# Kernel optimization log

Measured on AMD Instinct MI355X. Metric: run time of the kernel, lower is better.

The kernel has to match this reference:

```python
import jax, jax.numpy as jnp
import numpy as np

THRESHOLD = 0.3          # config.sparse_threshold
COMPETITION_FACTOR = 2.0 # config.competition_factor
TARGET_SPARSITY = 0.1    # config.target_sparsity


def setup_inputs() -> dict:
    key = jax.random.key(0)
    B, D = 32768, 1024
    H = D // 4
    ks = jax.random.split(key, 18)
    def lin(k, fan_in, shape):
        return jax.random.normal(k, shape, dtype=jnp.float32) / np.sqrt(fan_in)
    return {
        "features": jax.random.normal(ks[0], (B, D), dtype=jnp.float32),
        # sparse_gating: Linear(D, D//4) -> ReLU -> Linear(D//4, D) -> Sigmoid
        "w_g1": lin(ks[1], D, (D, H)), "b_g1": jnp.zeros((H,), jnp.float32),
        "w_g2": lin(ks[2], H, (H, D)), "b_g2": jnp.zeros((D,), jnp.float32),
        # competition_calculator: Linear(D, D) -> ReLU -> Linear(D, 1) -> Sigmoid
        "w_c1": lin(ks[3], D, (D, D)), "b_c1": jnp.zeros((D,), jnp.float32),
        "w_c2": lin(ks[4], D, (D, 1)), "b_c2": jnp.zeros((1,), jnp.float32),
        # sparsity_feedback: Linear(2, 16) -> ReLU -> Linear(16, D) -> Sigmoid
        "w_r1": lin(ks[5], 2, (2, 16)), "b_r1": jnp.zeros((16,), jnp.float32),
        "w_r2": lin(ks[6], 16, (16, D)), "b_r2": jnp.zeros((D,), jnp.float32),
        # adaptive_threshold: Linear(3, 16) -> ReLU -> Linear(16, 1) -> Sigmoid
        "w_m1": lin(ks[7], 3, (3, 16)), "b_m1": jnp.zeros((16,), jnp.float32),
        "w_m2": lin(ks[8], 16, (16, 1)), "b_m2": jnp.zeros((1,), jnp.float32),
    }


def _competitive_sparse(f, w_c1, b_c1, w_c2, b_c2):
    # competition_strength: [B, 1] scalar per row (output Linear has out_dim 1)
    c = jax.nn.sigmoid(jax.nn.relu(f @ w_c1 + b_c1) @ w_c2 + b_c2)  # [B,1]
    inh = COMPETITION_FACTOR * c                                     # [B,1]
    # other_activations_j = f_j * (1 - inh) for j != i, and f_i at position i.
    scaled = f * (1.0 - inh)                                         # [B,D]
    # max over j != i of scaled_j, vectorized via top-2
    top2_vals, _ = jax.lax.top_k(scaled, 2)                          # [B,2]
    am = jnp.argmax(scaled, axis=-1)                                 # [B]
    idx = jnp.arange(f.shape[-1])
    max_excl = jnp.where(idx[None, :] == am[:, None],
                         top2_vals[:, 1:2], top2_vals[:, 0:1])       # [B,D]
    other_max = jnp.maximum(f, max_excl)                             # includes own f_i term
    win = other_max < f
    return jnp.where(f > THRESHOLD, jnp.where(win, f, 0.0), f)


def reference(features, w_g1, b_g1, w_g2, b_g2, w_c1, b_c1, w_c2, b_c2,
              w_r1, b_r1, w_r2, b_r2, w_m1, b_m1, w_m2, b_m2):
    # 1) sparse gating
    gw = jax.nn.sigmoid(jax.nn.relu(features @ w_g1 + b_g1) @ w_g2 + b_g2)
    gated = features * gw
    # 2) competitive sparse activation
    comp = _competitive_sparse(gated, w_c1, b_c1, w_c2, b_c2)
    # 3) dynamic sparsity regulation
    cur_sp = jnp.mean((jnp.abs(comp) < 0.1).astype(comp.dtype), axis=-1)  # [B]
    sp_in = jnp.stack([cur_sp, jnp.full_like(cur_sp, TARGET_SPARSITY)], axis=-1)  # [B,2]
    rw = jax.nn.sigmoid(jax.nn.relu(sp_in @ w_r1 + b_r1) @ w_r2 + b_r2)  # [B,D]
    dyn = comp * rw
    # 4) adaptive threshold (monitor); torch.std is unbiased -> ddof=1
    fmean = jnp.mean(dyn, axis=-1, keepdims=True)
    fstd = jnp.std(dyn, axis=-1, ddof=1, keepdims=True)
    fmax = jnp.max(dyn, axis=-1, keepdims=True)
    thr_in = jnp.concatenate([fmean, fstd, fmax], axis=-1)            # [B,3]
    thr = jax.nn.sigmoid(jax.nn.relu(thr_in @ w_m1 + b_m1) @ w_m2 + b_m2)  # [B,1]
    # 5) final sparse mask
    mask = (jnp.abs(dyn) > thr).astype(dyn.dtype)
    return dyn * mask
```

## Files before the change

### kernel.cpp

```cpp
#include <hip/hip_runtime.h>
#include <cmath>

#define TM 128
#define TN 128
#define TK 16
#define LDSW 132
#define FIXCAP  262144u
#define FIXCAP2 131072u
#define ROWCAP 32768u

#define B03  2.5e-5f
#define B01  2.5e-5f
#define B2   5e-6
#define BDYN 3e-5f

typedef __attribute__((ext_vector_type(8))) short bf16x8;
typedef __attribute__((ext_vector_type(8))) unsigned short ushort8;
typedef __attribute__((ext_vector_type(4))) float f32x4;

__device__ __forceinline__ unsigned short bf16_rne(float x)
{
    unsigned u = __float_as_uint(x);
    unsigned r = u + 0x7FFFu + ((u >> 16) & 1u);
    return (unsigned short)(r >> 16);
}
__device__ __forceinline__ float bf16_to_f(unsigned short h)
{
    return __uint_as_float(((unsigned)h) << 16);
}

#define STAGE_STORE(B)                                                          \
        As[B][aq * 4 + 0][ar] = pa0.x; As[B][aq * 4 + 1][ar] = pa0.y;           \
        As[B][aq * 4 + 2][ar] = pa0.z; As[B][aq * 4 + 3][ar] = pa0.w;           \
        As[B][aq * 4 + 0][ar + 64] = pa1.x; As[B][aq * 4 + 1][ar + 64] = pa1.y; \
        As[B][aq * 4 + 2][ar + 64] = pa1.z; As[B][aq * 4 + 3][ar + 64] = pa1.w; \
        *(float4*)&Bs[B][bk][bn4] = pb0;                                        \
        *(float4*)&Bs[B][bk + 8][bn4] = pb1;

#define GEMM_MAINLOOP(Aptr, Wptr, Kdim, Ndim)                                   \
    __shared__ float As[2][TK][LDSW];                                           \
    __shared__ float Bs[2][TK][LDSW];                                           \
    const int tid = threadIdx.x;                                                \
    const int bm = blockIdx.x * TM;                                             \
    const int bn = blockIdx.y * TN;                                             \
    const int tx = tid & 15, ty = tid >> 4;                                     \
    const int ar = tid >> 2, aq = tid & 3;                                      \
    const int bk = tid >> 5, bn4 = (tid & 31) * 4;                              \
    float acc[2][2][4][4];                                                      \
    _Pragma("unroll") for (int a = 0; a < 2; ++a)                               \
    _Pragma("unroll") for (int b = 0; b < 2; ++b)                               \
    _Pragma("unroll") for (int i = 0; i < 4; ++i)                               \
    _Pragma("unroll") for (int j = 0; j < 4; ++j) acc[a][b][i][j] = 0.f;        \
    float4 pa0 = *(const float4*)((Aptr) + (size_t)(bm + ar) * (Kdim) + aq * 4);      \
    float4 pa1 = *(const float4*)((Aptr) + (size_t)(bm + ar + 64) * (Kdim) + aq * 4); \
    float4 pb0 = *(const float4*)((Wptr) + (size_t)bk * (Ndim) + bn + bn4);           \
    float4 pb1 = *(const float4*)((Wptr) + (size_t)(bk + 8) * (Ndim) + bn + bn4);     \
    STAGE_STORE(0)                                                              \
    __syncthreads();                                                            \
    int buf = 0;                                                                \
    for (int k0 = 0; k0 < (Kdim); k0 += TK) {                                   \
        const int nk = k0 + TK;                                                 \
        if (nk < (Kdim)) {                                                      \
            pa0 = *(const float4*)((Aptr) + (size_t)(bm + ar) * (Kdim) + nk + aq * 4);      \
            pa1 = *(const float4*)((Aptr) + (size_t)(bm + ar + 64) * (Kdim) + nk + aq * 4); \
            pb0 = *(const float4*)((Wptr) + (size_t)(nk + bk) * (Ndim) + bn + bn4);         \
            pb1 = *(const float4*)((Wptr) + (size_t)(nk + bk + 8) * (Ndim) + bn + bn4);     \
        }                                                                       \
        _Pragma("unroll") for (int k = 0; k < TK; ++k) {                        \
            float4 da0 = *(const float4*)&As[buf][k][ty * 4];                   \
            float4 da1 = *(const float4*)&As[buf][k][64 + ty * 4];              \
            float4 db0 = *(const float4*)&Bs[buf][k][tx * 4];                   \
            float4 db1 = *(const float4*)&Bs[buf][k][64 + tx * 4];              \
            const float* dap[2] = {&da0.x, &da1.x};                             \
            const float* dbp[2] = {&db0.x, &db1.x};                             \
            _Pragma("unroll") for (int a = 0; a < 2; ++a)                       \
            _Pragma("unroll") for (int b = 0; b < 2; ++b)                       \
            _Pragma("unroll") for (int i = 0; i < 4; ++i)                       \
            _Pragma("unroll") for (int j = 0; j < 4; ++j)                       \
                acc[a][b][i][j] = fmaf(dap[a][i], dbp[b][j], acc[a][b][i][j]);  \
        }                                                                       \
        if (nk < (Kdim)) {                                                      \
            const int nb = buf ^ 1;                                             \
            STAGE_STORE(nb)                                                     \
            __syncthreads();                                                    \
            buf = nb;                                                           \
        }                                                                       \
    }

__global__ __launch_bounds__(256) void gemm1_f32(
    const float* __restrict__ A, const float* __restrict__ W,
    const float* __restrict__ bias, float* __restrict__ out, int M)
{
    const int K = 1024, N = 256;
    GEMM_MAINLOOP(A, W, K, N)
    #pragma unroll
    for (int a = 0; a < 2; ++a) {
        #pragma unroll
        for (int b = 0; b < 2; ++b) {
            const int col = bn + b * 64 + tx * 4;
            float4 bi = *(const float4*)(bias + col);
            #pragma unroll
            for (int i = 0; i < 4; ++i) {
                const int row = bm + a * 64 + ty * 4 + i;
                float4 o;
                o.x = fmaxf(acc[a][b][i][0] + bi.x, 0.f);
                o.y = fmaxf(acc[a][b][i][1] + bi.y, 0.f);
                o.z = fmaxf(acc[a][b][i][2] + bi.z, 0.f);
                o.w = fmaxf(acc[a][b][i][3] + bi.w, 0.f);
                *(float4*)(out + (size_t)row * N + col) = o;
            }
        }
    }
}

__global__ __launch_bounds__(256) void split_wg2(
    const float* __restrict__ wg2, unsigned short* __restrict__ th,
    unsigned short* __restrict__ tl)
{
    const int n = blockIdx.x;
    const int k = threadIdx.x;
    float x = wg2[(size_t)k * 1024 + n];
    unsigned short h = bf16_rne(x);
    th[(size_t)n * 256 + k] = h;
    tl[(size_t)n * 256 + k] = bf16_rne(x - bf16_to_f(h));
}

__global__ __launch_bounds__(256) void gemm2_mfma(
    const float* __restrict__ h1, const unsigned short* __restrict__ bTh,
    const unsigned short* __restrict__ bTl, const float* __restrict__ bias,
    const float* __restrict__ F, float* __restrict__ out,
    unsigned* __restrict__ ectr1, uint2* __restrict__ elist1, int M)
{
    __shared__ __align__(16) unsigned short Ah[128][40];
    __shared__ __align__(16) unsigned short Al[128][40];
    __shared__ __align__(16) unsigned short Bh[128][40];
    __shared__ __align__(16) unsigned short Bl[128][40];

    const int tid  = threadIdx.x;
    const int lane = tid & 63;
    const int wave = tid >> 6;
    const int wr = wave >> 1, wc = wave & 1;
    const int bm = blockIdx.x * 128;
    const int bn = blockIdx.y * 128;

    f32x4 acc[4][4];
    #pragma unroll
    for (int mi = 0; mi < 4; ++mi)
        #pragma unroll
        for (int ni = 0; ni < 4; ++ni)
            acc[mi][ni] = (f32x4){0.f, 0.f, 0.f, 0.f};

    const int sr = tid >> 1;
    const int sh = tid & 1;

    for (int k0 = 0; k0 < 256; k0 += 32) {
        __syncthreads();
        {
            const float* src = h1 + (size_t)(bm + sr) * 256 + k0 + sh * 16;
            unsigned short* dh = &Ah[sr][sh * 16];
            unsigned short* dl = &Al[sr][sh * 16];
            #pragma unroll
            for (int i = 0; i < 2; ++i) {
                float4 f0 = ((const float4*)src)[2 * i + 0];
                float4 f1 = ((const float4*)src)[2 * i + 1];
                float xs[8] = {f0.x, f0.y, f0.z, f0.w, f1.x, f1.y, f1.z, f1.w};
                ushort8 vh, vl;
                #pragma unroll
                for (int j = 0; j < 8; ++j) {
                    unsigned short hh = bf16_rne(xs[j]);
                    vh[j] = hh;
                    vl[j] = bf16_rne(xs[j] - bf16_to_f(hh));
                }
                ((ushort8*)dh)[i] = vh;
                ((ushort8*)dl)[i] = vl;
            }
        }
        {
            const ushort8* s0 = (const ushort8*)(bTh + (size_t)(bn + sr) * 256 + k0 + sh * 16);
            const ushort8* s1 = (const ushort8*)(bTl + (size_t)(bn + sr) * 256 + k0 + sh * 16);
            ushort8* d0 = (ushort8*)&Bh[sr][sh * 16];
            ushort8* d1 = (ushort8*)&Bl[sr][sh * 16];
            d0[0] = s0[0]; d0[1] = s0[1];
            d1[0] = s1[0]; d1[1] = s1[1];
        }
        __syncthreads();

        const int ko = (lane >> 4) * 8;
        const int fr = lane & 15;
        bf16x8 ah[4], al[4], bh[4], bl[4];
        #pragma unroll
        for (int mi = 0; mi < 4; ++mi) {
            ah[mi] = *(const bf16x8*)&Ah[wr * 64 + mi * 16 + fr][ko];
            al[mi] = *(const bf16x8*)&Al[wr * 64 + mi * 16 + fr][ko];
        }
        #pragma unroll
        for (int ni = 0; ni < 4; ++ni) {
            bh[ni] = *(const bf16x8*)&Bh[wc * 64 + ni * 16 + fr][ko];
            bl[ni] = *(const bf16x8*)&Bl[wc * 64 + ni * 16 + fr][ko];
        }
        #pragma unroll
        for (int mi = 0; mi < 4; ++mi) {
            #pragma unroll
            for (int ni = 0; ni < 4; ++ni) {
                acc[mi][ni] = __builtin_amdgcn_mfma_f32_16x16x32_bf16(ah[mi], bh[ni], acc[mi][ni], 0, 0, 0);
                acc[mi][ni] = __builtin_amdgcn_mfma_f32_16x16x32_bf16(ah[mi], bl[ni], acc[mi][ni], 0, 0, 0);
                acc[mi][ni] = __builtin_amdgcn_mfma_f32_16x16x32_bf16(al[mi], bh[ni], acc[mi][ni], 0, 0, 0);
            }
        }
    }

    #pragma unroll
    for (int ni = 0; ni < 4; ++ni) {
        const int col = bn + wc * 64 + ni * 16 + (lane & 15);
        const float bi = bias[col];
        #pragma unroll
        for (int mi = 0; mi < 4; ++mi) {
            #pragma unroll
            for (int r = 0; r < 4; ++r) {
                const int row = bm + wr * 64 + mi * 16 + (lane >> 4) * 4 + r;
                float z = acc[mi][ni][r] + bi;
                float gw = 1.0f / (1.0f + __expf(-z));
                float g = F[(size_t)row * 1024 + col] * gw;
                float c = (g > 0.3f) ? 0.f : g;
                if (fabsf(g - 0.3f) < B03 || fabsf(fabsf(c) - 0.1f) < B01) {
                    unsigned idx = atomicAdd(ectr1, 1u);
                    if (idx < FIXCAP) elist1[idx] = make_uint2((unsigned)row, (unsigned)col);
                }
                out[(size_t)row * 1024 + col] = c;
            }
        }
    }
}

__global__ __launch_bounds__(256) void fix_near(
    const float* __restrict__ h1, const float* __restrict__ F,
    const float* __restrict__ Wg2, const float* __restrict__ bg2,
    const unsigned* __restrict__ ectr1, const uint2* __restrict__ elist1,
    unsigned* __restrict__ ectr2, uint2* __restrict__ elist2,
    float* __restrict__ out, int* __restrict__ corr)
{
    __shared__ double red[4];
    const int tid = threadIdx.x;
    unsigned cnt = *ectr1;
    if (cnt > FIXCAP) cnt = FIXCAP;

    for (unsigned e = blockIdx.x; e < cnt; e += gridDim.x) {
        const unsigned row = elist1[e].x, col = elist1[e].y;
        double p = (double)h1[(size_t)row * 256 + tid]
                 * (double)Wg2[(size_t)tid * 1024 + col];
        #pragma unroll
        for (int o = 32; o > 0; o >>= 1) p += __shfl_down(p, o, 64);
        if ((tid & 63) == 0) red[tid >> 6] = p;
        __syncthreads();
        if (tid == 0) {
            double z2 = red[0] + red[1] + red[2] + red[3] + (double)bg2[col];
            double gw = 1.0 / (1.0 + exp(-z2));
            double g = (double)F[(size_t)row * 1024 + col] * gw;
            double c = (g > 0.3) ? 0.0 : g;
            bool near = (fabs(g - 0.3) < B2) || (fabs(fabs(c) - 0.1) < B2);
            if (near) {
                unsigned i2 = atomicAdd(ectr2, 1u);
                if (i2 < FIXCAP2) elist2[i2] = make_uint2(row, col);
            } else {
                float cf = (float)c;
                int d_ref = (fabs(c) < 0.1) ? 1 : 0;
                int d_st  = (fabsf(cf) < 0.1f) ? 1 : 0;
                if (d_ref != d_st) atomicAdd(&corr[row], d_ref - d_st);
                out[(size_t)row * 1024 + col] = cf;
            }
        }
        __syncthreads();
    }
}

#define WT_PREFETCH(ptr)                                                        \
            r0 = *(const float4*)((ptr) + 0 * 1024 + tid * 4);                  \
            r1 = *(const float4*)((ptr) + 1 * 1024 + tid * 4);                  \
            r2 = *(const float4*)((ptr) + 2 * 1024 + tid * 4);                  \
            r3 = *(const float4*)((ptr) + 3 * 1024 + tid * 4);

#define WT_STORE(B)                                                             \
            *(float4*)&Wt[B][0 * 1024 + tid * 4] = r0;                          \
            *(float4*)&Wt[B][1 * 1024 + tid * 4] = r1;                          \
            *(float4*)&Wt[B][2 * 1024 + tid * 4] = r2;                          \
            *(float4*)&Wt[B][3 * 1024 + tid * 4] = r3;

__global__ __launch_bounds__(256) void fix_full(
    const float* __restrict__ F, const float* __restrict__ Wg1,
    const float* __restrict__ bg1, const float* __restrict__ Wg2,
    const float* __restrict__ bg2,
    const unsigned* __restrict__ ectr2, const uint2* __restrict__ elist2,
    float* __restrict__ out, int* __restrict__ corr)
{
    __shared__ float Fs[1024];
    __shared__ float Wt[2][4096];
    __shared__ double red[4];
    const int tid = threadIdx.x;
    unsigned cnt = *ectr2;
    if (cnt > FIXCAP2) cnt = FIXCAP2;

    for (unsigned e = blockIdx.x; e < cnt; e += gridDim.x) {
        const unsigned row = elist2[e].x, col = elist2[e].y;
        __syncthreads();
        *(float4*)&Fs[tid * 4] = *(const float4*)(F + (size_t)row * 1024 + tid * 4);

        float4 r0, r1, r2, r3;
        WT_PREFETCH(Wg1)
        WT_STORE(0)
        __syncthreads();
        double p0 = 0.0, p1 = 0.0, p2 = 0.0, p3 = 0.0;
        int buf = 0;
        for (int t = 0; t < 64; ++t) {
            if (t + 1 < 64) { const float* np = Wg1 + (size_t)(t + 1) * 4096; WT_PREFETCH(np) }
            const int kb = t * 16;
            #pragma unroll
            for (int kk = 0; kk < 16; kk += 4) {
                p0 += (double)Fs[kb + kk + 0] * (double)Wt[buf][(kk + 0) * 256 + tid];
                p1 += (double)Fs[kb + kk + 1] * (double)Wt[buf][(kk + 1) * 256 + tid];
                p2 += (double)Fs[kb + kk + 2] * (double)Wt[buf][(kk + 2) * 256 + tid];
                p3 += (double)Fs[kb + kk + 3] * (double)Wt[buf][(kk + 3) * 256 + tid];
            }
            if (t + 1 < 64) {
                const int nb = buf ^ 1;
                WT_STORE(nb)
                __syncthreads();
                buf = nb;
            }
        }
        double h = ((p0 + p1) + (p2 + p3)) + (double)bg1[tid];
        h = (h > 0.0) ? h : 0.0;
        double p = h * (double)Wg2[(size_t)tid * 1024 + col];
        #pragma unroll
        for (int o = 32; o > 0; o >>= 1) p += __shfl_down(p, o, 64);
        if ((tid & 63) == 0) red[tid >> 6] = p;
        __syncthreads();
        if (tid == 0) {
            double z2 = red[0] + red[1] + red[2] + red[3] + (double)bg2[col];
            double gw = 1.0 / (1.0 + exp(-z2));
            double g = (double)Fs[col] * gw;
            double c = (g > 0.3) ? 0.0 : g;
            float cf = (float)c;
            int d_ref = (fabs(c) < 0.1) ? 1 : 0;
            int d_st  = (fabsf(cf) < 0.1f) ? 1 : 0;
            if (d_ref != d_st) atomicAdd(&corr[row], d_ref - d_st);
            out[(size_t)row * 1024 + col] = cf;
        }
    }
}

__global__ __launch_bounds__(256) void finalize_rows(
    float* __restrict__ C,
    const float* __restrict__ wr1, const float* __restrict__ br1,
    const float* __restrict__ wr2, const float* __restrict__ br2,
    const float* __restrict__ wm1, const float* __restrict__ bm1,
    const float* __restrict__ wm2, const float* __restrict__ bm2,
    const int* __restrict__ corr,
    unsigned* __restrict__ rctr, unsigned* __restrict__ rowlist)
{
    const int D = 1024;
    const int tid = threadIdx.x;
    const int lane = tid & 63;
    const unsigned row = blockIdx.x * 4 + (tid >> 6);
    const size_t base = (size_t)row * D;
    const int col0 = lane * 4;

    float4 c4[4];
    #pragma unroll
    for (int q = 0; q < 4; ++q)
        c4[q] = *(const float4*)(C + base + q * 256 + col0);

    float c[16];
    #pragma unroll
    for (int q = 0; q < 4; ++q) {
        c[q * 4 + 0] = c4[q].x; c[q * 4 + 1] = c4[q].y;
        c[q * 4 + 2] = c4[q].z; c[q * 4 + 3] = c4[q].w;
    }

    float cnt = 0.f;
    #pragma unroll
    for (int i = 0; i < 16; ++i) cnt += (fabsf(c[i]) < 0.1f) ? 1.f : 0.f;
    #pragma unroll
    for (int o = 32; o > 0; o >>= 1) cnt += __shfl_xor(cnt, o, 64);
    cnt += (float)corr[row];
    const double cur_sp = (double)cnt / 1024.0;

    float hid[16];
    #pragma unroll
    for (int h = 0; h < 16; ++h) {
        double z = cur_sp * (double)wr1[h] + 0.1 * (double)wr1[16 + h] + (double)br1[h];
        hid[h] = (float)((z > 0.0) ? z : 0.0);
    }

    float dyn[16];
    #pragma unroll
    for (int q = 0; q < 4; ++q) {
        const int cq = q * 256 + col0;
        float4 b4 = *(const float4*)(br2 + cq);
        float z[4] = {b4.x, b4.y, b4.z, b4.w};
        #pragma unroll
        for (int h = 0; h < 16; ++h) {
            float4 w4 = *(const float4*)(wr2 + (size_t)h * D + cq);
            z[0] = fmaf(hid[h], w4.x, z[0]);
            z[1] = fmaf(hid[h], w4.y, z[1]);
            z[2] = fmaf(hid[h], w4.z, z[2]);
            z[3] = fmaf(hid[h], w4.w, z[3]);
        }
        #pragma unroll
        for (int j = 0; j < 4; ++j) {
            float rw = 1.0f / (1.0f + __expf(-z[j]));
            dyn[q * 4 + j] = c[q * 4 + j] * rw;
        }
    }

    float s = 0.f, mx = -1e30f;
    #pragma unroll
    for (int i = 0; i < 16; ++i) { s += dyn[i]; mx = fmaxf(mx, dyn[i]); }
    #pragma unroll
    for (int o = 32; o > 0; o >>= 1) s += __shfl_xor(s, o, 64);
    const float mean = s / 1024.0f;

    float sq = 0.f;
    #pragma unroll
    for (int i = 0; i < 16; ++i) { float d = dyn[i] - mean; sq = fmaf(d, d, sq); }
    #pragma unroll
    for (int o = 32; o > 0; o >>= 1) sq += __shfl_xor(sq, o, 64);
    const float sd = sqrtf(sq / 1023.0f);

    #pragma unroll
    for (int o = 32; o > 0; o >>= 1) mx = fmaxf(mx, __shfl_xor(mx, o, 64));

    double acc2 = (double)bm2[0];
    #pragma unroll
    for (int h = 0; h < 16; ++h) {
        double hz = (double)mean * (double)wm1[h] + (double)sd * (double)wm1[16 + h]
                  + (double)mx * (double)wm1[32 + h] + (double)bm1[h];
        hz = (hz > 0.0) ? hz : 0.0;
        acc2 += hz * (double)wm2[h];
    }
    const float thr = (float)(1.0 / (1.0 + exp(-acc2)));

    bool fl = false;
    #pragma unroll
    for (int i = 0; i < 16; ++i)
        if (fabsf(fabsf(dyn[i]) - thr) < BDYN) fl = true;

    if (__any(fl)) {
        if (lane == 0) {
            unsigned idx = atomicAdd(rctr, 1u);
            if (idx < ROWCAP) rowlist[idx] = row;
        }
        return;
    }

    #pragma unroll
    for (int q = 0; q < 4; ++q) {
        float4 o4;
        float* op = &o4.x;
        #pragma unroll
        for (int j = 0; j < 4; ++j) {
            float d = dyn[q * 4 + j];
            op[j] = (fabsf(d) > thr) ? d : 0.f;
        }
        *(float4*)(C + base + q * 256 + col0) = o4;
    }
}

__device__ __forceinline__ double block_reduce_d(double v, double* sm, int tid, int op)
{
    #pragma unroll
    for (int o = 32; o > 0; o >>= 1) {
        double other = __shfl_down(v, o, 64);
        v = op ? fmax(v, other) : (v + other);
    }
    if ((tid & 63) == 0) sm[tid >> 6] = v;
    __syncthreads();
    if (tid == 0) {
        double r = sm[0];
        for (int w = 1; w < 4; ++w) r = op ? fmax(r, sm[w]) : (r + sm[w]);
        sm[4] = r;
    }
    __syncthreads();
    double r = sm[4];
    __syncthreads();
    return r;
}

__global__ __launch_bounds__(256) void row_exact(
    const float* __restrict__ F,
    const float* __restrict__ wg1, const float* __restrict__ bg1,
    const float* __restrict__ wg2, const float* __restrict__ bg2,
    const float* __restrict__ wr1, const float* __restrict__ br1,
    const float* __restrict__ wr2, const float* __restrict__ br2,
    const float* __restrict__ wm1, const float* __restrict__ bm1,
    const float* __restrict__ wm2, const float* __restrict__ bm2,
    const unsigned* __restrict__ rctr, const unsigned* __restrict__ rowlist,
    float* __restrict__ out)
{
    __shared__ float  Fs[1024];
    __shared__ float  Wt[2][4096];
    __shared__ double h1d[256];
    __shared__ double sm[8];
    const int tid = threadIdx.x;
    unsigned rcnt = *rctr;
    if (rcnt > ROWCAP) rcnt = ROWCAP;

    for (unsigned e = blockIdx.x; e < rcnt; e += gridDim.x) {
        const unsigned row = rowlist[e];
        __syncthreads();
        *(float4*)&Fs[tid * 4] = *(const float4*)(F + (size_t)row * 1024 + tid * 4);

        {
            float4 r0, r1, r2, r3;
            WT_PREFETCH(wg1)
            WT_STORE(0)
            __syncthreads();
            double p0 = 0.0, p1 = 0.0, p2 = 0.0, p3 = 0.0;
            int buf = 0;
            for (int t = 0; t < 64; ++t) {
                if (t + 1 < 64) { const float* np = wg1 + (size_t)(t + 1) * 4096; WT_PREFETCH(np) }
                const int kb = t * 16;
                #pragma unroll
                for (int kk = 0; kk < 16; kk += 4) {
                    p0 += (double)Fs[kb + kk + 0] * (double)Wt[buf][(kk + 0) * 256 + tid];
                    p1 += (double)Fs[kb + kk + 1] * (double)Wt[buf][(kk + 1) * 256 + tid];
                    p2 += (double)Fs[kb + kk + 2] * (double)Wt[buf][(kk + 2) * 256 + tid];
                    p3 += (double)Fs[kb + kk + 3] * (double)Wt[buf][(kk + 3) * 256 + tid];
                }
                if (t + 1 < 64) {
                    const int nb = buf ^ 1;
                    WT_STORE(nb)
                    __syncthreads();
                    buf = nb;
                }
            }
            double a = ((p0 + p1) + (p2 + p3)) + (double)bg1[tid];
            h1d[tid] = (a > 0.0) ? a : 0.0;
        }
        __syncthreads();

        const int c0 = tid * 4;
        double zA[4] = {0.0, 0.0, 0.0, 0.0};
        double zB[4] = {0.0, 0.0, 0.0, 0.0};
        {
            float4 r0, r1, r2, r3;
            WT_PREFETCH(wg2)
            WT_STORE(0)
            __syncthreads();
            int buf = 0;
            for (int t = 0; t < 64; ++t) {
                if (t + 1 < 64) { const float* np = wg2 + (size_t)(t + 1) * 4096; WT_PREFETCH(np) }
                const int jb = t * 4;
                #pragma unroll
                for (int kk = 0; kk < 4; kk += 2) {
                    float4 wA = *(const float4*)&Wt[buf][(kk + 0) * 1024 + c0];
                    float4 wB = *(const float4*)&Wt[buf][(kk + 1) * 1024 + c0];
                    double hA = h1d[jb + kk], hB = h1d[jb + kk + 1];
                    zA[0] += hA * (double)wA.x; zA[1] += hA * (double)wA.y;
                    zA[2] += hA * (double)wA.z; zA[3] += hA * (double)wA.w;
                    zB[0] += hB * (double)wB.x; zB[1] += hB * (double)wB.y;
                    zB[2] += hB * (double)wB.z; zB[3] += hB * (double)wB.w;
                }
                if (t + 1 < 64) {
                    const int nb = buf ^ 1;
                    WT_STORE(nb)
                    __syncthreads();
                    buf = nb;
                }
            }
        }
        double comp[4];
        double cnt = 0.0;
        #pragma unroll
        for (int j = 0; j < 4; ++j) {
            double z2v = (double)bg2[c0 + j] + zA[j] + zB[j];
            double gw = 1.0 / (1.0 + exp(-z2v));
            double g = (double)Fs[c0 + j] * gw;
            double cm = (g > 0.3) ? 0.0 : g;
            comp[j] = cm;
            cnt += (fabs(cm) < 0.1) ? 1.0 : 0.0;
        }
        cnt = block_reduce_d(cnt, sm, tid, 0);
        const double cur_sp = cnt / 1024.0;

        double hid[16];
        #pragma unroll
        for (int h = 0; h < 16; ++h) {
            double hz = cur_sp * (double)wr1[h] + 0.1 * (double)wr1[16 + h] + (double)br1[h];
            hid[h] = (hz > 0.0) ? hz : 0.0;
        }
        double zr[4] = {(double)br2[c0], (double)br2[c0 + 1],
                        (double)br2[c0 + 2], (double)br2[c0 + 3]};
        #pragma unroll
        for (int h = 0; h < 16; ++h) {
            float4 w4 = *(const float4*)(wr2 + (size_t)h * 1024 + c0);
            zr[0] += hid[h] * (double)w4.x; zr[1] += hid[h] * (double)w4.y;
            zr[2] += hid[h] * (double)w4.z; zr[3] += hid[h] * (double)w4.w;
        }
        double dyn[4];
        #pragma unroll
        for (int j = 0; j < 4; ++j) {
            double rw = 1.0 / (1.0 + exp(-zr[j]));
            dyn[j] = comp[j] * rw;
        }

        double s = dyn[0] + dyn[1] + dyn[2] + dyn[3];
        s = block_reduce_d(s, sm, tid, 0);
        const double mean = s / 1024.0;

        double sq = 0.0;
        #pragma unroll
        for (int j = 0; j < 4; ++j) { double d = dyn[j] - mean; sq += d * d; }
        sq = block_reduce_d(sq, sm, tid, 0);
        const double sd = sqrt(sq / 1023.0);

        double mx = fmax(fmax(dyn[0], dyn[1]), fmax(dyn[2], dyn[3]));
        mx = block_reduce_d(mx, sm, tid, 1);

        double acc2 = (double)bm2[0];
        #pragma unroll
        for (int h = 0; h < 16; ++h) {
            double hz = mean * (double)wm1[h] + sd * (double)wm1[16 + h]
                      + mx * (double)wm1[32 + h] + (double)bm1[h];
            hz = (hz > 0.0) ? hz : 0.0;
            acc2 += hz * (double)wm2[h];
        }
        const double thr = 1.0 / (1.0 + exp(-acc2));

        float4 o4;
        o4.x = (float)((fabs(dyn[0]) > thr) ? dyn[0] : 0.0);
        o4.y = (float)((fabs(dyn[1]) > thr) ? dyn[1] : 0.0);
        o4.z = (float)((fabs(dyn[2]) > thr) ? dyn[2] : 0.0);
        o4.w = (float)((fabs(dyn[3]) > thr) ? dyn[3] : 0.0);
        *(float4*)(out + (size_t)row * 1024 + c0) = o4;
    }
}

extern "C" void kernel_launch(void* const* d_in, const int* in_sizes, int n_in,
                              void* d_out, int out_size, void* d_ws, size_t ws_size,
                              hipStream_t stream)
{
    const float* F   = (const float*)d_in[0];
    const float* wg1 = (const float*)d_in[1];
    const float* bg1 = (const float*)d_in[2];
    const float* wg2 = (const float*)d_in[3];
    const float* bg2 = (const float*)d_in[4];
    const float* wr1 = (const float*)d_in[9];
    const float* br1 = (const float*)d_in[10];
    const float* wr2 = (const float*)d_in[11];
    const float* br2 = (const float*)d_in[12];
    const float* wm1 = (const float*)d_in[13];
    const float* bm1 = (const float*)d_in[14];
    const float* wm2 = (const float*)d_in[15];
    const float* bm2 = (const float*)d_in[16];

    float* out = (float*)d_out;
    const int M = in_sizes[0] / 1024;

    char* ws = (char*)d_ws;
    float*          h1      = (float*)ws;
    uint2*          elist1  = (uint2*)(ws + (32u << 20));
    unsigned short* wg2Th   = (unsigned short*)(ws + (34u << 20));
    unsigned short* wg2Tl   = (unsigned short*)(ws + (34u << 20) + (512u << 10));
    uint2*          elist2  = (uint2*)(ws + (35u << 20));
    unsigned*       rowlist = (unsigned*)(ws + (36u << 20));
    int*            corr    = (int*)(ws + (36u << 20) + (128u << 10));
    unsigned*       ctrs    = (unsigned*)(ws + (36u << 20) + (256u << 10));
    unsigned* ectr1 = ctrs, *ectr2 = ctrs + 1, *rctr = ctrs + 2;

    hipMemsetAsync(corr, 0, (size_t)M * sizeof(int) + 16, stream);
    split_wg2<<<1024, 256, 0, stream>>>(wg2, wg2Th, wg2Tl);
    gemm1_f32<<<dim3(M / TM, 256 / TN), 256, 0, stream>>>(F, wg1, bg1, h1, M);
    gemm2_mfma<<<dim3(M / 128, 1024 / 128), 256, 0, stream>>>(h1, wg2Th, wg2Tl, bg2, F,
                                                              out, ectr1, elist1, M);
    fix_near<<<2048, 256, 0, stream>>>(h1, F, wg2, bg2, ectr1, elist1, ectr2, elist2, out, corr);
    fix_full<<<1024, 256, 0, stream>>>(F, wg1, bg1, wg2, bg2, ectr2, elist2, out, corr);
    finalize_rows<<<M / 4, 256, 0, stream>>>(out, wr1, br1, wr2, br2, wm1, bm1, wm2, bm2,
                                             corr, rctr, rowlist);
    row_exact<<<2048, 256, 0, stream>>>(F, wg1, bg1, wg2, bg2, wr1, br1, wr2, br2,
                                        wm1, bm1, wm2, bm2, rctr, rowlist, out);
}
```

Baseline: 909.0 us.

## Replace fp32 SIMT first gating GEMM with split-bf16 MFMA GEMM

The first gating GEMM (features x w_g1) moves from a scalar fp32 FMA tiled kernel to MFMA bf16 instructions. It uses a hi/lo split of both operands with three MFMA passes to approximate fp32 accuracy. A new kernel pre-splits and transposes w_g1 into bf16 hi/lo buffers placed in workspace shared with the later error list. The error-bound constants for the near-threshold fixup paths are widened to absorb the extra rounding error, which may push more elements into the correction kernels.

```diff
diff --git a/kernel.cpp b/kernel.cpp
--- a/kernel.cpp
+++ b/kernel.cpp
@@ -1,18 +1,14 @@
 #include <hip/hip_runtime.h>
 #include <cmath>
 
-#define TM 128
-#define TN 128
-#define TK 16
-#define LDSW 132
 #define FIXCAP  262144u
 #define FIXCAP2 131072u
 #define ROWCAP 32768u
 
-#define B03  2.5e-5f
-#define B01  2.5e-5f
-#define B2   5e-6
-#define BDYN 3e-5f
+#define B03  4e-5f
+#define B01  4e-5f
+#define B2   2e-5
+#define BDYN 5e-5f
 
 typedef __attribute__((ext_vector_type(8))) short bf16x8;
 typedef __attribute__((ext_vector_type(8))) unsigned short ushort8;
@@ -29,87 +25,18 @@
     return __uint_as_float(((unsigned)h) << 16);
 }
 
-#define STAGE_STORE(B)                                                          \
-        As[B][aq * 4 + 0][ar] = pa0.x; As[B][aq * 4 + 1][ar] = pa0.y;           \
-        As[B][aq * 4 + 2][ar] = pa0.z; As[B][aq * 4 + 3][ar] = pa0.w;           \
-        As[B][aq * 4 + 0][ar + 64] = pa1.x; As[B][aq * 4 + 1][ar + 64] = pa1.y; \
-        As[B][aq * 4 + 2][ar + 64] = pa1.z; As[B][aq * 4 + 3][ar + 64] = pa1.w; \
-        *(float4*)&Bs[B][bk][bn4] = pb0;                                        \
-        *(float4*)&Bs[B][bk + 8][bn4] = pb1;
-
-#define GEMM_MAINLOOP(Aptr, Wptr, Kdim, Ndim)                                   \
-    __shared__ float As[2][TK][LDSW];                                           \
-    __shared__ float Bs[2][TK][LDSW];                                           \
-    const int tid = threadIdx.x;                                                \
-    const int bm = blockIdx.x * TM;                                             \
-    const int bn = blockIdx.y * TN;                                             \
-    const int tx = tid & 15, ty = tid >> 4;                                     \
-    const int ar = tid >> 2, aq = tid & 3;                                      \
-    const int bk = tid >> 5, bn4 = (tid & 31) * 4;                              \
-    float acc[2][2][4][4];                                                      \
-    _Pragma("unroll") for (int a = 0; a < 2; ++a)                               \
-    _Pragma("unroll") for (int b = 0; b < 2; ++b)                               \
-    _Pragma("unroll") for (int i = 0; i < 4; ++i)                               \
-    _Pragma("unroll") for (int j = 0; j < 4; ++j) acc[a][b][i][j] = 0.f;        \
-    float4 pa0 = *(const float4*)((Aptr) + (size_t)(bm + ar) * (Kdim) + aq * 4);      \
-    float4 pa1 = *(const float4*)((Aptr) + (size_t)(bm + ar + 64) * (Kdim) + aq * 4); \
-    float4 pb0 = *(const float4*)((Wptr) + (size_t)bk * (Ndim) + bn + bn4);           \
-    float4 pb1 = *(const float4*)((Wptr) + (size_t)(bk + 8) * (Ndim) + bn + bn4);     \
-    STAGE_STORE(0)                                                              \
-    __syncthreads();                                                            \
-    int buf = 0;                                                                \
-    for (int k0 = 0; k0 < (Kdim); k0 += TK) {                                   \
-        const int nk = k0 + TK;                                                 \
-        if (nk < (Kdim)) {                                                      \
-            pa0 = *(const float4*)((Aptr) + (size_t)(bm + ar) * (Kdim) + nk + aq * 4);      \
-            pa1 = *(const float4*)((Aptr) + (size_t)(bm + ar + 64) * (Kdim) + nk + aq * 4); \
-            pb0 = *(const float4*)((Wptr) + (size_t)(nk + bk) * (Ndim) + bn + bn4);         \
-            pb1 = *(const float4*)((Wptr) + (size_t)(nk + bk + 8) * (Ndim) + bn + bn4);     \
-        }                                                                       \
-        _Pragma("unroll") for (int k = 0; k < TK; ++k) {                        \
-            float4 da0 = *(const float4*)&As[buf][k][ty * 4];                   \
-            float4 da1 = *(const float4*)&As[buf][k][64 + ty * 4];              \
-            float4 db0 = *(const float4*)&Bs[buf][k][tx * 4];                   \
-            float4 db1 = *(const float4*)&Bs[buf][k][64 + tx * 4];              \
-            const float* dap[2] = {&da0.x, &da1.x};                             \
-            const float* dbp[2] = {&db0.x, &db1.x};                             \
-            _Pragma("unroll") for (int a = 0; a < 2; ++a)                       \
-            _Pragma("unroll") for (int b = 0; b < 2; ++b)                       \
-            _Pragma("unroll") for (int i = 0; i < 4; ++i)                       \
-            _Pragma("unroll") for (int j = 0; j < 4; ++j)                       \
-                acc[a][b][i][j] = fmaf(dap[a][i], dbp[b][j], acc[a][b][i][j]);  \
-        }                                                                       \
-        if (nk < (Kdim)) {                                                      \
-            const int nb = buf ^ 1;                                             \
-            STAGE_STORE(nb)                                                     \
-            __syncthreads();                                                    \
-            buf = nb;                                                           \
-        }                                                                       \
-    }
-
-__global__ __launch_bounds__(256) void gemm1_f32(
-    const float* __restrict__ A, const float* __restrict__ W,
-    const float* __restrict__ bias, float* __restrict__ out, int M)
-{
-    const int K = 1024, N = 256;
-    GEMM_MAINLOOP(A, W, K, N)
-    #pragma unroll
-    for (int a = 0; a < 2; ++a) {
-        #pragma unroll
-        for (int b = 0; b < 2; ++b) {
-            const int col = bn + b * 64 + tx * 4;
-            float4 bi = *(const float4*)(bias + col);
-            #pragma unroll
-            for (int i = 0; i < 4; ++i) {
-                const int row = bm + a * 64 + ty * 4 + i;
-                float4 o;
-                o.x = fmaxf(acc[a][b][i][0] + bi.x, 0.f);
-                o.y = fmaxf(acc[a][b][i][1] + bi.y, 0.f);
-                o.z = fmaxf(acc[a][b][i][2] + bi.z, 0.f);
-                o.w = fmaxf(acc[a][b][i][3] + bi.w, 0.f);
-                *(float4*)(out + (size_t)row * N + col) = o;
-            }
-        }
+__global__ __launch_bounds__(256) void split_wg1(
+    const float* __restrict__ wg1, unsigned short* __restrict__ th,
+    unsigned short* __restrict__ tl)
+{
+    const int n = blockIdx.x;
+    #pragma unroll
+    for (int kc = 0; kc < 4; ++kc) {
+        const int k = kc * 256 + threadIdx.x;
+        float x = wg1[(size_t)k * 256 + n];
+        unsigned short h = bf16_rne(x);
+        th[(size_t)n * 1024 + k] = h;
+        tl[(size_t)n * 1024 + k] = bf16_rne(x - bf16_to_f(h));
     }
 }
 
@@ -123,6 +50,104 @@
     unsigned short h = bf16_rne(x);
     th[(size_t)n * 256 + k] = h;
     tl[(size_t)n * 256 + k] = bf16_rne(x - bf16_to_f(h));
+}
+
+__global__ __launch_bounds__(256) void gemm1_mfma(
+    const float* __restrict__ F, const unsigned short* __restrict__ bTh,
+    const unsigned short* __restrict__ bTl, const float* __restrict__ bias,
+    float* __restrict__ out, int M)
+{
+    __shared__ __align__(16) unsigned short Ah[128][40];
+    __shared__ __align__(16) unsigned short Al[128][40];
+    __shared__ __align__(16) unsigned short Bh[128][40];
+    __shared__ __align__(16) unsigned short Bl[128][40];
+
+    const int tid  = threadIdx.x;
+    const int lane = tid & 63;
+    const int wave = tid >> 6;
+    const int wr = wave >> 1, wc = wave & 1;
+    const int bm = blockIdx.x * 128;
+    const int bn = blockIdx.y * 128;
+
+    f32x4 acc[4][4];
+    #pragma unroll
+    for (int mi = 0; mi < 4; ++mi)
+        #pragma unroll
+        for (int ni = 0; ni < 4; ++ni)
+            acc[mi][ni] = (f32x4){0.f, 0.f, 0.f, 0.f};
+
+    const int sr = tid >> 1;
+    const int sh = tid & 1;
+
+    for (int k0 = 0; k0 < 1024; k0 += 32) {
+        __syncthreads();
+        {
+            const float* src = F + (size_t)(bm + sr) * 1024 + k0 + sh * 16;
+            unsigned short* dh = &Ah[sr][sh * 16];
+            unsigned short* dl = &Al[sr][sh * 16];
+            #pragma unroll
+            for (int i = 0; i < 2; ++i) {
+                float4 f0 = ((const float4*)src)[2 * i + 0];
+                float4 f1 = ((const float4*)src)[2 * i + 1];
+                float xs[8] = {f0.x, f0.y, f0.z, f0.w, f1.x, f1.y, f1.z, f1.w};
+                ushort8 vh, vl;
+                #pragma unroll
+                for (int j = 0; j < 8; ++j) {
+                    unsigned short hh = bf16_rne(xs[j]);
+                    vh[j] = hh;
+                    vl[j] = bf16_rne(xs[j] - bf16_to_f(hh));
+                }
+                ((ushort8*)dh)[i] = vh;
+                ((ushort8*)dl)[i] = vl;
+            }
+        }
+        {
+            const ushort8* s0 = (const ushort8*)(bTh + (size_t)(bn + sr) * 1024 + k0 + sh * 16);
+            const ushort8* s1 = (const ushort8*)(bTl + (size_t)(bn + sr) * 1024 + k0 + sh * 16);
+            ushort8* d0 = (ushort8*)&Bh[sr][sh * 16];
+            ushort8* d1 = (ushort8*)&Bl[sr][sh * 16];
+            d0[0] = s0[0]; d0[1] = s0[1];
+            d1[0] = s1[0]; d1[1] = s1[1];
+        }
+        __syncthreads();
+
+        const int ko = (lane >> 4) * 8;
+        const int fr = lane & 15;
+        bf16x8 ah[4], al[4], bh[4], bl[4];
+        #pragma unroll
+        for (int mi = 0; mi < 4; ++mi) {
+            ah[mi] = *(const bf16x8*)&Ah[wr * 64 + mi * 16 + fr][ko];
+            al[mi] = *(const bf16x8*)&Al[wr * 64 + mi * 16 + fr][ko];
+        }
+        #pragma unroll
+        for (int ni = 0; ni < 4; ++ni) {
+            bh[ni] = *(const bf16x8*)&Bh[wc * 64 + ni * 16 + fr][ko];
+            bl[ni] = *(const bf16x8*)&Bl[wc * 64 + ni * 16 + fr][ko];
+        }
+        #pragma unroll
+        for (int mi = 0; mi < 4; ++mi) {
+            #pragma unroll
+            for (int ni = 0; ni < 4; ++ni) {
+                acc[mi][ni] = __builtin_amdgcn_mfma_f32_16x16x32_bf16(ah[mi], bh[ni], acc[mi][ni], 0, 0, 0);
+                acc[mi][ni] = __builtin_amdgcn_mfma_f32_16x16x32_bf16(ah[mi], bl[ni], acc[mi][ni], 0, 0, 0);
+                acc[mi][ni] = __builtin_amdgcn_mfma_f32_16x16x32_bf16(al[mi], bh[ni], acc[mi][ni], 0, 0, 0);
+            }
+        }
+    }
+
+    #pragma unroll
+    for (int ni = 0; ni < 4; ++ni) {
+        const int col = bn + wc * 64 + ni * 16 + (lane & 15);
+        const float bi = bias[col];
+        #pragma unroll
+        for (int mi = 0; mi < 4; ++mi) {
+            #pragma unroll
+            for (int r = 0; r < 4; ++r) {
+                const int row = bm + wr * 64 + mi * 16 + (lane >> 4) * 4 + r;
+                out[(size_t)row * 256 + col] = fmaxf(acc[mi][ni][r] + bi, 0.f);
+            }
+        }
+    }
 }
 
 __global__ __launch_bounds__(256) void gemm2_mfma(
@@ -658,6 +683,8 @@
 
     char* ws = (char*)d_ws;
     float*          h1      = (float*)ws;
+    unsigned short* wg1Th   = (unsigned short*)(ws + (32u << 20));
+    unsigned short* wg1Tl   = (unsigned short*)(ws + (32u << 20) + (512u << 10));
     uint2*          elist1  = (uint2*)(ws + (32u << 20));
     unsigned short* wg2Th   = (unsigned short*)(ws + (34u << 20));
     unsigned short* wg2Tl   = (unsigned short*)(ws + (34u << 20) + (512u << 10));
@@ -668,8 +695,9 @@
     unsigned* ectr1 = ctrs, *ectr2 = ctrs + 1, *rctr = ctrs + 2;
 
     hipMemsetAsync(corr, 0, (size_t)M * sizeof(int) + 16, stream);
+    split_wg1<<<256, 256, 0, stream>>>(wg1, wg1Th, wg1Tl);
     split_wg2<<<1024, 256, 0, stream>>>(wg2, wg2Th, wg2Tl);
-    gemm1_f32<<<dim3(M / TM, 256 / TN), 256, 0, stream>>>(F, wg1, bg1, h1, M);
+    gemm1_mfma<<<dim3(M / 128, 256 / 128), 256, 0, stream>>>(F, wg1Th, wg1Tl, bg1, h1, M);
     gemm2_mfma<<<dim3(M / 128, 1024 / 128), 256, 0, stream>>>(h1, wg2Th, wg2Tl, bg2, F,
                                                               out, ectr1, elist1, M);
     fix_near<<<2048, 256, 0, stream>>>(h1, F, wg2, bg2, ectr1, elist1, ectr2, elist2, out, corr);
```

Measured after the change: 1.070 ms. 17.7% more time.
